# Kernel optimization log

Hardware: AMD Instinct MI355X
Metric: run time of the kernel (lower is better)

The kernel has to match this reference:

```python
import jax, jax.numpy as jnp
import numpy as np

B, M, D, H = 2, 2048, 1024, 16
DH = D // H            # 64 head dim
R_ATTN = 512           # rank of q/k/v SVD factors
FFN_D = 2048           # GEGLU inner dim; Wi out = 2*FFN_D
R_FFN = 1024           # rank of FFN SVD factors
ROPE_BASE = 10000.0
LN_EPS = 1e-5


def _layernorm(x, g, b):
    mu = jnp.mean(x, axis=-1, keepdims=True)
    var = jnp.mean(jnp.square(x - mu), axis=-1, keepdims=True)
    return (x - mu) * jax.lax.rsqrt(var + LN_EPS) * g + b


def _rotate_half(x):
    x1, x2 = jnp.split(x, 2, axis=-1)
    return jnp.concatenate((-x2, x1), axis=-1)


def _rope_cos_sin(m, dh, dtype):
    inv_freq = 1.0 / (ROPE_BASE ** (jnp.arange(0, dh, 2, dtype=jnp.float32) / dh))
    freqs = jnp.arange(m, dtype=jnp.float32)[:, None] * inv_freq[None, :]  # [M, dh/2]
    emb = jnp.concatenate((freqs, freqs), axis=-1)  # [M, dh]
    return jnp.cos(emb).astype(dtype), jnp.sin(emb).astype(dtype)


def setup_inputs() -> dict:
    key = jax.random.key(0)
    ks = iter(jax.random.split(key, 32))
    rn = lambda shape, s: jax.random.normal(next(ks), shape, jnp.float32) * s
    w = 0.02
    return {
        'hidden_states': rn((B, M, D), 1.0),
        'ln1_g': jnp.ones((D,), jnp.float32), 'ln1_b': jnp.zeros((D,), jnp.float32),
        'Uq': rn((D, R_ATTN), w), 'Vq': rn((R_ATTN, D), w), 'bq': rn((D,), w),
        'Uk': rn((D, R_ATTN), w), 'Vk': rn((R_ATTN, D), w), 'bk': rn((D,), w),
        'Uv': rn((D, R_ATTN), w), 'Vv': rn((R_ATTN, D), w), 'bv': rn((D,), w),
        'Wo': rn((D, D), w), 'bo': rn((D,), w),  # dense attn out proj, torch [out,in]
        'ln2_g': jnp.ones((D,), jnp.float32), 'ln2_b': jnp.zeros((D,), jnp.float32),
        'U1': rn((D, R_FFN), w), 'V1': rn((R_FFN, 2 * FFN_D), w), 'b1': rn((2 * FFN_D,), w),
        'U2': rn((FFN_D, R_FFN), w), 'V2': rn((R_FFN, D), w), 'b2': rn((D,), w),
    }


def reference(hidden_states, ln1_g, ln1_b, Uq, Vq, bq, Uk, Vk, bk, Uv, Vv, bv,
              Wo, bo, ln2_g, ln2_b, U1, V1, b1, U2, V2, b2):
    x = hidden_states
    xn = _layernorm(x, ln1_g, ln1_b)
    # low-rank QKV: y = (x @ U) @ V + b
    q = (xn @ Uq) @ Vq + bq
    k = (xn @ Uk) @ Vk + bk
    v = (xn @ Uv) @ Vv + bv
    to_bhmd = lambda t: t.reshape(B, M, H, DH).transpose(0, 2, 1, 3)
    q, k, v = to_bhmd(q), to_bhmd(k), to_bhmd(v)
    cos, sin = _rope_cos_sin(M, DH, q.dtype)  # [M, DH]
    q = q * cos + _rotate_half(q) * sin
    k = k * cos + _rotate_half(k) * sin
    scale = 1.0 / np.sqrt(DH)
    scores = jnp.einsum('bhmd,bhnd->bhmn', q, k) * scale  # [B,H,M,M]
    attn = jax.nn.softmax(scores, axis=-1)
    out = jnp.einsum('bhmn,bhnd->bhmd', attn, v)
    out = out.transpose(0, 2, 1, 3).reshape(B, M, D)
    x = x + out @ Wo.T + bo
    # low-rank GEGLU FFN
    xn2 = _layernorm(x, ln2_g, ln2_b)
    z = (xn2 @ U1) @ V1 + b1  # [B,M,2*FFN_D]
    z1, z2 = jnp.split(z, 2, axis=-1)
    h = jax.nn.gelu(z1, approximate=True) * z2  # GEGLU, tanh approx
    y = (h @ U2) @ V2 + b2
    return x + y
```

## Files before the change

### kernel.cpp

```cpp
#include <hip/hip_runtime.h>


typedef unsigned short u16;
typedef unsigned int u32;
typedef u16 u16x8 __attribute__((ext_vector_type(8)));
typedef __bf16 bf16x8 __attribute__((ext_vector_type(8)));
typedef float f32x4 __attribute__((ext_vector_type(4)));

__device__ __forceinline__ u16 f2bf(float f) {
    u32 u = __builtin_bit_cast(u32, f);
    u += 0x7fff + ((u >> 16) & 1);
    return (u16)(u >> 16);
}
__device__ __forceinline__ float bf2f(u16 h) {
    u32 u = ((u32)h) << 16;
    return __builtin_bit_cast(float, u);
}
__device__ __forceinline__ u32 packbf(float a, float b) {
    return __builtin_amdgcn_perm(__builtin_bit_cast(u32, b),
                                 __builtin_bit_cast(u32, a), 0x07060302u);
}

__device__ __forceinline__ void gload16(const void* g, void* l) {
    __builtin_amdgcn_global_load_lds(
        (const __attribute__((address_space(1))) void*)g,
        (__attribute__((address_space(3))) void*)l, 16, 0, 0);
}

#define MB 1048576u
#define OFF_UQKVT (0*MB)
#define OFF_VQKVT (3*MB)
#define OFF_WOB   (6*MB)
#define OFF_U1T   (8*MB)
#define OFF_V1TP  (10*MB)
#define OFF_U2T   (18*MB)
#define OFF_V2T   (22*MB)
#define OFF_BQKV  (24*MB)
#define OFF_B1P   (24*MB + 16384u)
#define OFF_XN    (25*MB)
#define OFF_TBUF  (33*MB)
#define OFF_QB    (45*MB)
#define OFF_KB    (53*MB)
#define OFF_HB    (45*MB)
#define OFF_VTB   (61*MB)
#define OFF_OB    (69*MB)
#define OFF_X2    (93*MB)

__global__ __launch_bounds__(256) void prep_kernel(
    const float* __restrict__ Uq, const float* __restrict__ Uk,
    const float* __restrict__ Uv, const float* __restrict__ Vq,
    const float* __restrict__ Vk, const float* __restrict__ Vv,
    const float* __restrict__ Wo, const float* __restrict__ U1,
    const float* __restrict__ V1, const float* __restrict__ U2,
    const float* __restrict__ V2,
    const float* __restrict__ bq, const float* __restrict__ bk,
    const float* __restrict__ bv, const float* __restrict__ b1,
    u16* __restrict__ UQKVT, u16* __restrict__ VQKVT, u16* __restrict__ WOB,
    u16* __restrict__ U1T, u16* __restrict__ V1TP, u16* __restrict__ U2T,
    u16* __restrict__ V2T, float* __restrict__ BQKV, float* __restrict__ B1P)
{
    __shared__ float tile[32][33];
    int bid = blockIdx.x;

    if (bid >= 12288) {
        int id = (bid - 12288) * 256 + threadIdx.x;
        if (id < 3072) {
            float v = (id < 1024) ? bq[id] : (id < 2048 ? bk[id - 1024] : bv[id - 2048]);
            BQKV[id] = v;
        }
        int g = id >> 5, s = id & 31;
        B1P[id] = b1[(s < 16) ? (g*16 + s) : (2048 + g*16 + (s - 16))];
        return;
    }
    if (bid >= 11264) {
        int i4 = ((bid - 11264) * 256 + threadIdx.x) * 4;
        float4 v = *(const float4*)(Wo + i4);
        u16 tmp[4] = {f2bf(v.x), f2bf(v.y), f2bf(v.z), f2bf(v.w)};
        *(uint2*)(WOB + i4) = *(const uint2*)tmp;
        return;
    }

    const float* src; u16* dst; int K, N, src_ld, nx; bool gg = false;
    if (bid < 3072) {
        int t = bid / 512; bid -= t * 512;
        if (t < 3) { src = t==0 ? Uq : (t==1 ? Uk : Uv);
                     dst = UQKVT + t * 512*1024; K = 1024; N = 512; src_ld = 512; nx = 16; }
        else { int z = t - 3; src = z==0 ? Vq : (z==1 ? Vk : Vv);
               dst = VQKVT + z * 524288; K = 512; N = 1024; src_ld = 1024; nx = 32; }
    } else if (bid < 4096)  { src = U1; dst = U1T;  K = 1024; N = 1024; src_ld = 1024; nx = 32;  bid -= 3072; }
    else if (bid < 8192)    { src = V1; dst = V1TP; K = 1024; N = 4096; src_ld = 4096; nx = 128; bid -= 4096; gg = true; }
    else if (bid < 10240)   { src = U2; dst = U2T;  K = 2048; N = 1024; src_ld = 1024; nx = 32;  bid -= 8192; }
    else                    { src = V2; dst = V2T;  K = 1024; N = 1024; src_ld = 1024; nx = 32;  bid -= 10240; }

    int tx = threadIdx.x & 31, ty = threadIdx.x >> 5;
    int n0 = (bid % nx) * 32, k0 = (bid / nx) * 32;
    int srccol;
    if (gg) { int g = n0 >> 5; srccol = (tx < 16) ? (g*16 + tx) : (2048 + g*16 + (tx - 16)); }
    else srccol = n0 + tx;
    for (int i = 0; i < 4; i++)
        tile[ty + i*8][tx] = src[(size_t)(k0 + ty + i*8) * src_ld + srccol];
    __syncthreads();
    for (int i = 0; i < 4; i++)
        dst[(size_t)(n0 + ty + i*8) * K + k0 + tx] = f2bf(tile[tx][ty + i*8]);
}

__global__ __launch_bounds__(256) void ln_kernel(
    const float* __restrict__ x, const float* __restrict__ g,
    const float* __restrict__ bta, u16* __restrict__ out)
{
    int w = threadIdx.x >> 6, lane = threadIdx.x & 63;
    int row = blockIdx.x * 4 + w;
    const float* xr = x + (size_t)row * 1024;
    float vals[16];
    float s = 0.f, s2 = 0.f;
    #pragma unroll
    for (int ii = 0; ii < 16; ii++) {
        float v = xr[lane + ii*64];
        vals[ii] = v; s += v; s2 += v * v;
    }
    #pragma unroll
    for (int off = 1; off < 64; off <<= 1) {
        s  += __shfl_xor(s, off);
        s2 += __shfl_xor(s2, off);
    }
    float mu = s * (1.f/1024.f);
    float var = s2 * (1.f/1024.f) - mu * mu;
    float rs = rsqrtf(var + 1e-5f);
    #pragma unroll
    for (int ii = 0; ii < 16; ii++) {
        int col = lane + ii*64;
        out[(size_t)row * 1024 + col] = f2bf((vals[ii] - mu) * rs * g[col] + bta[col]);
    }
}

__global__ __launch_bounds__(256) void gemm_bt_kernel(
    const u16* __restrict__ A, int lda, const u16* __restrict__ Bt,
    void* __restrict__ Cout, int ldc, const float* __restrict__ bias,
    const float* __restrict__ resid, int Kdim, int mode)
{
    __shared__ u16 As[2][4096];
    __shared__ u16 Bs[2][4096];
    int tid = threadIdx.x;
    int m0 = blockIdx.y * 128, n0 = blockIdx.x * 128;
    int w = tid >> 6, lane = tid & 63, quad = lane >> 4, l15 = lane & 15;
    int wm = (w >> 1) * 64, wn = (w & 1) * 64;
    int sr = tid >> 2, sc8 = (tid & 3) * 8;

    f32x4 acc[4][4] = {};

    const u16* Ap = A  + (size_t)(m0 + sr) * lda  + sc8;
    const u16* Bp = Bt + (size_t)(n0 + sr) * Kdim + sc8;

    #define GSTAGE(buf, koff) do {                                        \
        gload16(Ap + (koff),                     &As[buf][tid * 8]);      \
        gload16(Ap + (koff) + (size_t)64 * lda,  &As[buf][2048 + tid*8]); \
        gload16(Bp + (koff),                     &Bs[buf][tid * 8]);      \
        gload16(Bp + (koff) + (size_t)64 * Kdim, &Bs[buf][2048 + tid*8]); \
    } while (0)

    GSTAGE(0, 0);
    __syncthreads();

    for (int k0 = 0; k0 < Kdim; k0 += 32) {
        int cur = (k0 >> 5) & 1;
        if (k0 + 32 < Kdim) GSTAGE(cur ^ 1, k0 + 32);
        const u16* Asc = As[cur];
        const u16* Bsc = Bs[cur];
        bf16x8 af[4], bfr[4];
        #pragma unroll
        for (int i = 0; i < 4; i++)
            af[i] = *(const bf16x8*)&Asc[(wm + i*16 + l15) * 32 + quad * 8];
        #pragma unroll
        for (int j = 0; j < 4; j++)
            bfr[j] = *(const bf16x8*)&Bsc[(wn + j*16 + l15) * 32 + quad * 8];
        #pragma unroll
        for (int i = 0; i < 4; i++)
            #pragma unroll
            for (int j = 0; j < 4; j++)
                acc[i][j] = __builtin_amdgcn_mfma_f32_16x16x32_bf16(af[i], bfr[j], acc[i][j], 0, 0, 0);
        __syncthreads();
    }
    #undef GSTAGE

    if (mode == 2) {
        u16* hb = (u16*)Cout;
        #pragma unroll
        for (int i = 0; i < 4; i++) {
            int row = m0 + wm + i*16 + quad*4;
            #pragma unroll
            for (int p = 0; p < 2; p++) {
                int colz = n0 + wn + p*32 + l15;
                float bz1 = bias[colz], bz2 = bias[colz + 16];
                int hcol = ((n0 + wn) >> 1) + p*16 + l15;
                #pragma unroll
                for (int r = 0; r < 4; r++) {
                    float z1 = acc[i][2*p][r] + bz1;
                    float z2 = acc[i][2*p+1][r] + bz2;
                    float uu = 0.7978845608028654f * (z1 + 0.044715f * z1 * z1 * z1);
                    float e = __expf(2.f * uu);
                    float th = (e - 1.f) / (e + 1.f);
                    float hv = 0.5f * z1 * (1.f + th) * z2;
                    hb[(size_t)(row + r) * ldc + hcol] = f2bf(hv);
                }
            }
        }
        return;
    }
    #pragma unroll
    for (int i = 0; i < 4; i++) {
        int row = m0 + wm + i*16 + quad*4;
        #pragma unroll
        for (int j = 0; j < 4; j++) {
            int col = n0 + wn + j*16 + l15;
            float bv = bias ? bias[col] : 0.f;
            #pragma unroll
            for (int r = 0; r < 4; r++) {
                float v = acc[i][j][r] + bv;
                size_t idx = (size_t)(row + r) * ldc + col;
                if (mode == 0) ((float*)Cout)[idx] = v + resid[idx];
                else           ((u16*)Cout)[idx] = f2bf(v);
            }
        }
    }
}

__global__ __launch_bounds__(256) void gemm_bt64_kernel(
    const u16* __restrict__ A, int lda, const u16* __restrict__ Bt,
    void* __restrict__ Cout, int ldc, const float* __restrict__ bias,
    const float* __restrict__ resid, int Kdim, int mode)
{
    __shared__ u16 As[2][4096];
    __shared__ u16 Bs[2][2048];
    int tid = threadIdx.x;
    int m0 = blockIdx.y * 128, n0 = blockIdx.x * 64;
    int w = tid >> 6, lane = tid & 63, quad = lane >> 4, l15 = lane & 15;
    int wm = (w >> 1) * 64, wn = (w & 1) * 32;
    int sr = tid >> 2, sc8 = (tid & 3) * 8;

    f32x4 acc[4][2] = {};

    const u16* Ap = A  + (size_t)(m0 + sr) * lda  + sc8;
    const u16* Bp = Bt + (size_t)(n0 + sr) * Kdim + sc8;

    #define GSTAGE64(buf, koff) do {                                       \
        gload16(Ap + (koff),                     &As[buf][tid * 8]);       \
        gload16(Ap + (koff) + (size_t)64 * lda,  &As[buf][2048 + tid*8]);  \
        gload16(Bp + (koff),                     &Bs[buf][tid * 8]);       \
    } while (0)

    GSTAGE64(0, 0);
    __syncthreads();

    for (int k0 = 0; k0 < Kdim; k0 += 32) {
        int cur = (k0 >> 5) & 1;
        if (k0 + 32 < Kdim) GSTAGE64(cur ^ 1, k0 + 32);
        const u16* Asc = As[cur];
        const u16* Bsc = Bs[cur];
        bf16x8 af[4], bfr[2];
        #pragma unroll
        for (int i = 0; i < 4; i++)
            af[i] = *(const bf16x8*)&Asc[(wm + i*16 + l15) * 32 + quad * 8];
        #pragma unroll
        for (int j = 0; j < 2; j++)
            bfr[j] = *(const bf16x8*)&Bsc[(wn + j*16 + l15) * 32 + quad * 8];
        #pragma unroll
        for (int i = 0; i < 4; i++)
            #pragma unroll
            for (int j = 0; j < 2; j++)
                acc[i][j] = __builtin_amdgcn_mfma_f32_16x16x32_bf16(af[i], bfr[j], acc[i][j], 0, 0, 0);
        __syncthreads();
    }
    #undef GSTAGE64

    #pragma unroll
    for (int i = 0; i < 4; i++) {
        int row = m0 + wm + i*16 + quad*4;
        #pragma unroll
        for (int j = 0; j < 2; j++) {
            int col = n0 + wn + j*16 + l15;
            float bv = bias ? bias[col] : 0.f;
            #pragma unroll
            for (int r = 0; r < 4; r++) {
                float v = acc[i][j][r] + bv;
                size_t idx = (size_t)(row + r) * ldc + col;
                if (mode == 0) ((float*)Cout)[idx] = v + resid[idx];
                else           ((u16*)Cout)[idx] = f2bf(v);
            }
        }
    }
}

__global__ __launch_bounds__(256) void qkv2_kernel(
    const u16* __restrict__ T, const u16* __restrict__ Vw,
    const float* __restrict__ bqkv, u16* __restrict__ qout,
    u16* __restrict__ kout, u16* __restrict__ vtout)
{
    __shared__ u16 As[2][4096];
    __shared__ u16 Bs[2][4096];
    int tid = threadIdx.x;
    int z = blockIdx.z;
    int m0 = blockIdx.y * 128, n0 = blockIdx.x * 128;
    int w = tid >> 6, lane = tid & 63, quad = lane >> 4, l15 = lane & 15;
    int wm = (w >> 1) * 64, wn = (w & 1) * 64;
    int sr = tid >> 2, sc8 = (tid & 3) * 8;

    f32x4 acc[4][4] = {};

    const u16* Ap = T  + (size_t)z * 512 + (size_t)(m0 + sr) * 1536 + sc8;
    const u16* Bp = Vw + (size_t)z * 512 * 1024 + (size_t)(n0 + sr) * 512 + sc8;

    #define QSTAGE(buf, koff) do {                                        \
        gload16(Ap + (koff),                     &As[buf][tid * 8]);      \
        gload16(Ap + (koff) + (size_t)64 * 1536, &As[buf][2048 + tid*8]); \
        gload16(Bp + (koff),                     &Bs[buf][tid * 8]);      \
        gload16(Bp + (koff) + (size_t)64 * 512,  &Bs[buf][2048 + tid*8]); \
    } while (0)

    QSTAGE(0, 0);
    __syncthreads();

    for (int k0 = 0; k0 < 512; k0 += 32) {
        int cur = (k0 >> 5) & 1;
        if (k0 + 32 < 512) QSTAGE(cur ^ 1, k0 + 32);
        const u16* Asc = As[cur];
        const u16* Bsc = Bs[cur];
        bf16x8 af[4], bfr[4];
        #pragma unroll
        for (int i = 0; i < 4; i++)
            af[i] = *(const bf16x8*)&Asc[(wm + i*16 + l15) * 32 + quad * 8];
        #pragma unroll
        for (int j = 0; j < 4; j++)
            bfr[j] = *(const bf16x8*)&Bsc[(wn + j*16 + l15) * 32 + quad * 8];
        #pragma unroll
        for (int i = 0; i < 4; i++)
            #pragma unroll
            for (int j = 0; j < 4; j++)
                acc[i][j] = __builtin_amdgcn_mfma_f32_16x16x32_bf16(af[i], bfr[j], acc[i][j], 0, 0, 0);
        __syncthreads();
    }
    #undef QSTAGE

    const float* bias = bqkv + z * 1024;
    if (z < 2) {
        u16* Ob = z ? kout : qout;
        float qscale = z ? 1.f : 0.18033688011112042f;
        #pragma unroll
        for (int i = 0; i < 4; i++) {
            int row0 = m0 + wm + i*16 + quad*4;
            #pragma unroll
            for (int j = 0; j < 2; j++) {
                int col = n0 + wn + j*16 + l15;
                float bj = bias[col], bj2 = bias[col + 32];
                float invf = exp2f((float)(col & 31) * -0.4152410118609203f);
                #pragma unroll
                for (int r = 0; r < 4; r++) {
                    int t = row0 + r;
                    float fr = (float)(t & 2047) * invf;
                    float sn, cs;
                    __sincosf(fr, &sn, &cs);
                    sn *= qscale; cs *= qscale;
                    float v1 = acc[i][j][r] + bj;
                    float v2 = acc[i][j+2][r] + bj2;
                    Ob[(size_t)t * 1024 + col]      = f2bf(v1 * cs - v2 * sn);
                    Ob[(size_t)t * 1024 + col + 32] = f2bf(v2 * cs + v1 * sn);
                }
            }
        }
    } else {
        int bb = m0 >> 11;
        #pragma unroll
        for (int i = 0; i < 4; i++) {
            int row0 = m0 + wm + i*16 + quad*4;
            #pragma unroll
            for (int j = 0; j < 4; j++) {
                int col = n0 + wn + j*16 + l15;
                float bj = bias[col];
                u16 pack[4];
                #pragma unroll
                for (int r = 0; r < 4; r++) pack[r] = f2bf(acc[i][j][r] + bj);
                size_t dst = ((size_t)(bb * 16 + (col >> 6)) * 64 + (col & 63)) * 2048 + (row0 & 2047);
                *(uint2*)&vtout[dst] = *(const uint2*)pack;
            }
        }
    }
}

__global__ __launch_bounds__(256) void attn_kernel(
    const u16* __restrict__ Q, const u16* __restrict__ K,
    const u16* __restrict__ Vt, u16* __restrict__ O)
{
    __shared__ u16 Ks[2][64 * 64];
    __shared__ u16 Vs[2][64 * 64];
    __shared__ u16 Ps[128 * 72];
    int tid = threadIdx.x;
    int bh = blockIdx.x;
    int b = bh >> 4, h = bh & 15;
    int m0 = blockIdx.y * 128;
    int w = tid >> 6, lane = tid & 63, quad = lane >> 4, l15 = lane & 15;
    int wm = w * 32;
    size_t qkbase = (size_t)b * 2048 * 1024 + h * 64;
    const u16* Vg = Vt + (size_t)bh * 64 * 2048;

    bf16x8 qf[2][2];
    #pragma unroll
    for (int i = 0; i < 2; i++)
        #pragma unroll
        for (int ks = 0; ks < 2; ks++)
            qf[i][ks] = *(const bf16x8*)(Q + qkbase +
                (size_t)(m0 + wm + i*16 + l15) * 1024 + ks*32 + quad*8);

    f32x4 oacc[2][4] = {};
    float lsum[2] = {};

    int r0 = tid >> 3, p = tid & 7;
    int c0 = (p ^ (r0 & 7)) * 8;
    int xsw = l15 & 7;

    #define STAGE(buf, key0) do {                                               \
        gload16(K + qkbase + (size_t)((key0) + r0) * 1024 + c0,                 \
                &Ks[buf][r0 * 64 + p * 8]);                                     \
        gload16(K + qkbase + (size_t)((key0) + r0 + 32) * 1024 + c0,            \
                &Ks[buf][(r0 + 32) * 64 + p * 8]);                              \
        gload16(Vg + (size_t)r0 * 2048 + (key0) + c0,                           \
                &Vs[buf][r0 * 64 + p * 8]);                                     \
        gload16(Vg + (size_t)(r0 + 32) * 2048 + (key0) + c0,                    \
                &Vs[buf][(r0 + 32) * 64 + p * 8]);                              \
    } while (0)

    STAGE(0, 0);
    __syncthreads();

    for (int kt = 0; kt < 32; kt++) {
        int cur = kt & 1;
        if (kt < 31) STAGE(cur ^ 1, (kt + 1) * 64);
        const u16* Ksc = Ks[cur];
        const u16* Vsc = Vs[cur];

        f32x4 sacc[4][2] = {};
        #pragma unroll
        for (int ks = 0; ks < 2; ks++) {
            bf16x8 kf[4];
            #pragma unroll
            for (int jj = 0; jj < 4; jj++)
                kf[jj] = *(const bf16x8*)&Ksc[(jj*16 + l15) * 64 + (((ks*4 + quad) ^ xsw) * 8)];
            #pragma unroll
            for (int jj = 0; jj < 4; jj++)
                #pragma unroll
                for (int i = 0; i < 2; i++)
                    sacc[jj][i] = __builtin_amdgcn_mfma_f32_16x16x32_bf16(kf[jj], qf[i][ks], sacc[jj][i], 0, 0, 0);
        }

        #pragma unroll
        for (int i = 0; i < 2; i++) {
            int prow = (wm + i*16 + l15) * 72 + quad*4;
            #pragma unroll
            for (int jj = 0; jj < 4; jj++) {
                float p0 = __builtin_amdgcn_exp2f(sacc[jj][i][0]);
                float p1 = __builtin_amdgcn_exp2f(sacc[jj][i][1]);
                float p2 = __builtin_amdgcn_exp2f(sacc[jj][i][2]);
                float p3 = __builtin_amdgcn_exp2f(sacc[jj][i][3]);
                lsum[i] += (p0 + p1) + (p2 + p3);
                uint2 pk; pk.x = packbf(p0, p1); pk.y = packbf(p2, p3);
                *(uint2*)&Ps[prow + jj*16] = pk;
            }
        }

        #pragma unroll
        for (int ks = 0; ks < 2; ks++) {
            bf16x8 pf[2], vf[4];
            #pragma unroll
            for (int i = 0; i < 2; i++)
                pf[i] = *(const bf16x8*)&Ps[(wm + i*16 + l15) * 72 + ks*32 + quad*8];
            #pragma unroll
            for (int j = 0; j < 4; j++)
                vf[j] = *(const bf16x8*)&Vsc[(j*16 + l15) * 64 + (((ks*4 + quad) ^ xsw) * 8)];
            #pragma unroll
            for (int i = 0; i < 2; i++)
                #pragma unroll
                for (int j = 0; j < 4; j++)
                    oacc[i][j] = __builtin_amdgcn_mfma_f32_16x16x32_bf16(pf[i], vf[j], oacc[i][j], 0, 0, 0);
        }
        __syncthreads();
    }
    #undef STAGE

    float inv[2][4];
    #pragma unroll
    for (int i = 0; i < 2; i++) {
        float s = lsum[i];
        s += __shfl_xor(s, 16);
        s += __shfl_xor(s, 32);
        #pragma unroll
        for (int r = 0; r < 4; r++)
            inv[i][r] = 1.f / __shfl(s, (lane & 48) | (quad*4 + r));
    }
    #pragma unroll
    for (int i = 0; i < 2; i++)
        #pragma unroll
        for (int r = 0; r < 4; r++) {
            int row = m0 + wm + i*16 + quad*4 + r;
            #pragma unroll
            for (int j = 0; j < 4; j++)
                O[qkbase + (size_t)row * 1024 + j*16 + l15] = f2bf(oacc[i][j][r] * inv[i][r]);
        }
}

extern "C" void kernel_launch(void* const* d_in, const int* in_sizes, int n_in,
                              void* d_out, int out_size, void* d_ws, size_t ws_size,
                              hipStream_t stream) {
    (void)in_sizes; (void)n_in; (void)out_size; (void)ws_size;
    const float* x     = (const float*)d_in[0];
    const float* ln1_g = (const float*)d_in[1];
    const float* ln1_b = (const float*)d_in[2];
    const float* Uq    = (const float*)d_in[3];
    const float* Vq    = (const float*)d_in[4];
    const float* bq    = (const float*)d_in[5];
    const float* Uk    = (const float*)d_in[6];
    const float* Vk    = (const float*)d_in[7];
    const float* bk    = (const float*)d_in[8];
    const float* Uv    = (const float*)d_in[9];
    const float* Vv    = (const float*)d_in[10];
    const float* bv    = (const float*)d_in[11];
    const float* Wo    = (const float*)d_in[12];
    const float* bo    = (const float*)d_in[13];
    const float* ln2_g = (const float*)d_in[14];
    const float* ln2_b = (const float*)d_in[15];
    const float* U1    = (const float*)d_in[16];
    const float* V1    = (const float*)d_in[17];
    const float* b1    = (const float*)d_in[18];
    const float* U2    = (const float*)d_in[19];
    const float* V2    = (const float*)d_in[20];
    const float* b2    = (const float*)d_in[21];
    float* out = (float*)d_out;
    char* ws = (char*)d_ws;

    u16* UQKVT = (u16*)(ws + OFF_UQKVT);
    u16* VQKVT = (u16*)(ws + OFF_VQKVT);
    u16* WOB   = (u16*)(ws + OFF_WOB);
    u16* U1T   = (u16*)(ws + OFF_U1T);
    u16* V1TP  = (u16*)(ws + OFF_V1TP);
    u16* U2T   = (u16*)(ws + OFF_U2T);
    u16* V2T   = (u16*)(ws + OFF_V2T);
    float* BQKV = (float*)(ws + OFF_BQKV);
    float* B1P  = (float*)(ws + OFF_B1P);
    u16* xn  = (u16*)(ws + OFF_XN);
    u16* tbuf= (u16*)(ws + OFF_TBUF);
    u16* qb  = (u16*)(ws + OFF_QB);
    u16* kb  = (u16*)(ws + OFF_KB);
    u16* vtb = (u16*)(ws + OFF_VTB);
    u16* ob  = (u16*)(ws + OFF_OB);
    u16* hb  = (u16*)(ws + OFF_HB);
    float* x2 = (float*)(ws + OFF_X2);

    prep_kernel<<<12304, 256, 0, stream>>>(
        Uq, Uk, Uv, Vq, Vk, Vv, Wo, U1, V1, U2, V2, bq, bk, bv, b1,
        UQKVT, VQKVT, WOB, U1T, V1TP, U2T, V2T, BQKV, B1P);

    ln_kernel<<<1024, 256, 0, stream>>>(x, ln1_g, ln1_b, xn);

    gemm_bt64_kernel<<<dim3(24, 32), 256, 0, stream>>>(xn, 1024, UQKVT, tbuf, 1536,
                                                       nullptr, nullptr, 1024, 1);
    qkv2_kernel<<<dim3(8, 32, 3), 256, 0, stream>>>(tbuf, VQKVT, BQKV, qb, kb, vtb);

    attn_kernel<<<dim3(32, 16), 256, 0, stream>>>(qb, kb, vtb, ob);

    gemm_bt64_kernel<<<dim3(16, 32), 256, 0, stream>>>(ob, 1024, WOB, x2, 1024,
                                                       bo, x, 1024, 0);
    ln_kernel<<<1024, 256, 0, stream>>>(x2, ln2_g, ln2_b, xn);

    gemm_bt64_kernel<<<dim3(16, 32), 256, 0, stream>>>(xn, 1024, U1T, tbuf, 1024,
                                                       nullptr, nullptr, 1024, 1);
    gemm_bt_kernel<<<dim3(32, 32), 256, 0, stream>>>(tbuf, 1024, V1TP, hb, 2048,
                                                     B1P, nullptr, 1024, 2);
    gemm_bt64_kernel<<<dim3(16, 32), 256, 0, stream>>>(hb, 2048, U2T, tbuf, 1024,
                                                       nullptr, nullptr, 2048, 1);
    gemm_bt64_kernel<<<dim3(16, 32), 256, 0, stream>>>(tbuf, 1024, V2T, out, 1024,
                                                       b2, x2, 1024, 0);
}
```

Measured before the change: 426.6 us.

## Triple-buffer GEMM LDS stages with partial vmcnt waits before barriers

Converts the three bf16 MFMA GEMM kernels from double to triple buffering, issuing global-to-LDS loads two k-steps ahead. The full __syncthreads is replaced with an inline s_waitcnt vmcnt(N) plus s_barrier, so only the older stage must land while the newest loads stay in flight. This is meant to hide global load latency in the main loop, at the cost of 50% more LDS per block, which may lower occupancy. The reliance on an exact vmcnt count is fragile if the compiler emits other vector memory ops in the loop.

Result: slower. 460.4 us (+7.9%).

```diff
diff --git a/kernel.cpp b/kernel.cpp
--- a/kernel.cpp
+++ b/kernel.cpp
@@ -26,6 +26,9 @@
         (const __attribute__((address_space(1))) void*)g,
         (__attribute__((address_space(3))) void*)l, 16, 0, 0);
 }
+
+#define PIPE_BARRIER(N) __asm__ volatile(                         \
+    "s_waitcnt vmcnt(" #N ") lgkmcnt(0)\n\ts_barrier" ::: "memory")
 
 #define MB 1048576u
 #define OFF_UQKVT (0*MB)
@@ -138,8 +141,8 @@
     void* __restrict__ Cout, int ldc, const float* __restrict__ bias,
     const float* __restrict__ resid, int Kdim, int mode)
 {
-    __shared__ u16 As[2][4096];
-    __shared__ u16 Bs[2][4096];
+    __shared__ u16 As[3][4096];
+    __shared__ u16 Bs[3][4096];
     int tid = threadIdx.x;
     int m0 = blockIdx.y * 128, n0 = blockIdx.x * 128;
     int w = tid >> 6, lane = tid & 63, quad = lane >> 4, l15 = lane & 15;
@@ -159,11 +162,14 @@
     } while (0)
 
     GSTAGE(0, 0);
-    __syncthreads();
-
-    for (int k0 = 0; k0 < Kdim; k0 += 32) {
-        int cur = (k0 >> 5) & 1;
-        if (k0 + 32 < Kdim) GSTAGE(cur ^ 1, k0 + 32);
+    GSTAGE(1, 32);
+    PIPE_BARRIER(4);
+
+    int kt = 0;
+    for (int k0 = 0; k0 < Kdim; k0 += 32, kt++) {
+        int cur = kt % 3;
+        bool st = (k0 + 64) < Kdim;
+        if (st) GSTAGE((kt + 2) % 3, k0 + 64);
         const u16* Asc = As[cur];
         const u16* Bsc = Bs[cur];
         bf16x8 af[4], bfr[4];
@@ -178,7 +184,10 @@
             #pragma unroll
             for (int j = 0; j < 4; j++)
                 acc[i][j] = __builtin_amdgcn_mfma_f32_16x16x32_bf16(af[i], bfr[j], acc[i][j], 0, 0, 0);
-        __syncthreads();
+        if (k0 + 32 < Kdim) {
+            if (st) PIPE_BARRIER(4);
+            else    PIPE_BARRIER(0);
+        }
     }
     #undef GSTAGE
 
@@ -229,8 +238,8 @@
     void* __restrict__ Cout, int ldc, const float* __restrict__ bias,
     const float* __restrict__ resid, int Kdim, int mode)
 {
-    __shared__ u16 As[2][4096];
-    __shared__ u16 Bs[2][2048];
+    __shared__ u16 As[3][4096];
+    __shared__ u16 Bs[3][2048];
     int tid = threadIdx.x;
     int m0 = blockIdx.y * 128, n0 = blockIdx.x * 64;
     int w = tid >> 6, lane = tid & 63, quad = lane >> 4, l15 = lane & 15;
@@ -249,11 +258,14 @@
     } while (0)
 
     GSTAGE64(0, 0);
-    __syncthreads();
-
-    for (int k0 = 0; k0 < Kdim; k0 += 32) {
-        int cur = (k0 >> 5) & 1;
-        if (k0 + 32 < Kdim) GSTAGE64(cur ^ 1, k0 + 32);
+    GSTAGE64(1, 32);
+    PIPE_BARRIER(3);
+
+    int kt = 0;
+    for (int k0 = 0; k0 < Kdim; k0 += 32, kt++) {
+        int cur = kt % 3;
+        bool st = (k0 + 64) < Kdim;
+        if (st) GSTAGE64((kt + 2) % 3, k0 + 64);
         const u16* Asc = As[cur];
         const u16* Bsc = Bs[cur];
         bf16x8 af[4], bfr[2];
@@ -268,7 +280,10 @@
             #pragma unroll
             for (int j = 0; j < 2; j++)
                 acc[i][j] = __builtin_amdgcn_mfma_f32_16x16x32_bf16(af[i], bfr[j], acc[i][j], 0, 0, 0);
-        __syncthreads();
+        if (k0 + 32 < Kdim) {
+            if (st) PIPE_BARRIER(3);
+            else    PIPE_BARRIER(0);
+        }
     }
     #undef GSTAGE64
 
@@ -295,8 +310,8 @@
     const float* __restrict__ bqkv, u16* __restrict__ qout,
     u16* __restrict__ kout, u16* __restrict__ vtout)
 {
-    __shared__ u16 As[2][4096];
-    __shared__ u16 Bs[2][4096];
+    __shared__ u16 As[3][4096];
+    __shared__ u16 Bs[3][4096];
     int tid = threadIdx.x;
     int z = blockIdx.z;
     int m0 = blockIdx.y * 128, n0 = blockIdx.x * 128;
@@ -317,11 +332,14 @@
     } while (0)
 
     QSTAGE(0, 0);
-    __syncthreads();
-
-    for (int k0 = 0; k0 < 512; k0 += 32) {
-        int cur = (k0 >> 5) & 1;
-        if (k0 + 32 < 512) QSTAGE(cur ^ 1, k0 + 32);
+    QSTAGE(1, 32);
+    PIPE_BARRIER(4);
+
+    int kt = 0;
+    for (int k0 = 0; k0 < 512; k0 += 32, kt++) {
+        int cur = kt % 3;
+        bool st = (k0 + 64) < 512;
+        if (st) QSTAGE((kt + 2) % 3, k0 + 64);
         const u16* Asc = As[cur];
         const u16* Bsc = Bs[cur];
         bf16x8 af[4], bfr[4];
@@ -336,7 +354,10 @@
             #pragma unroll
             for (int j = 0; j < 4; j++)
                 acc[i][j] = __builtin_amdgcn_mfma_f32_16x16x32_bf16(af[i], bfr[j], acc[i][j], 0, 0, 0);
-        __syncthreads();
+        if (k0 + 32 < 512) {
+            if (st) PIPE_BARRIER(4);
+            else    PIPE_BARRIER(0);
+        }
     }
     #undef QSTAGE
 
```
